# Kernel tuning notes

Measured on AMD Instinct MI355X. Metric: run time of the kernel, lower is better.

Reference implementation:

```python
import jax, jax.numpy as jnp
import numpy as np

N = 50000        # nodes
E = 500000       # edges
NUM = 4          # sampled intermediate neighbors per edge (self.num)
F = 64           # in_feats == out_feats (transform=False)
D = 32           # dist_dim
NB = 64          # embedding rows = len(boundaries)+1


def setup_inputs() -> dict:
    key = jax.random.key(0)
    ks = jax.random.split(key, 10)
    feat = jax.random.normal(ks[0], (N, F), jnp.float32)
    loc = jax.random.uniform(ks[1], (N, 3), jnp.float32)          # 3D positions in unit cube
    boundaries = jnp.sort(jax.random.uniform(ks[2], (NB - 1,), jnp.float32, 0.0, 2.0))
    embed_table = jax.random.normal(ks[3], (NB, D), jnp.float32)
    G_w = jax.random.normal(ks[4], (F, D), jnp.float32) / np.sqrt(D)      # Linear(dist_dim->out, no bias)
    agg_w = jax.random.normal(ks[5], (F, 2 * F), jnp.float32) / np.sqrt(2 * F)  # Linear(2*out->out)
    agg_b = jnp.zeros((F,), jnp.float32)
    src = jax.random.randint(ks[6], (E,), 0, N, jnp.int32)
    dst = jax.random.randint(ks[7], (E,), 0, N, jnp.int32)
    inter_ids = jax.random.randint(ks[8], (E, NUM), 0, N, jnp.int32)
    return dict(feat=feat, loc=loc, boundaries=boundaries, embed_table=embed_table,
                G_w=G_w, agg_w=agg_w, agg_b=agg_b, src=src, dst=dst, inter_ids=inter_ids)


def reference(feat, loc, boundaries, embed_table, G_w, agg_w, agg_b, src, dst, inter_ids):
    n = feat.shape[0]
    ones = jnp.ones((src.shape[0],), feat.dtype)
    # symmetric-ish degree normalization: d0 = in_deg^-0.5, d2 = out_deg^-0.5
    in_deg = jax.ops.segment_sum(ones, dst, num_segments=n)
    out_deg = jax.ops.segment_sum(ones, src, num_segments=n)
    d0 = jnp.clip(in_deg, 1.0) ** -0.5   # [N]
    d2 = jnp.clip(out_deg, 1.0) ** -0.5  # [N]

    # dist1 = ||loc[dst] - loc[src]||_2, bucketize -> embed -> G
    dist1 = jnp.linalg.norm(loc[dst] - loc[src], axis=1)              # [E]
    de1 = embed_table[jnp.searchsorted(boundaries, dist1)] @ G_w.T    # [E, F]

    # intermediate sampled neighbors: dist to each sampled node from edge src
    pos_src = loc[src]                                                # [E, 3]
    inter_pos = loc[inter_ids]                                        # [E, NUM, 3]
    dist_ = jnp.linalg.norm(pos_src[:, None, :] - inter_pos, axis=-1) # [E, NUM]
    de_ = embed_table[jnp.searchsorted(boundaries, dist_)] @ G_w.T    # [E, NUM, F]
    inter_h = feat[inter_ids]                                         # [E, NUM, F]
    dist_embed_dot_h = (de_ * inter_h).mean(axis=1)                   # [E, F]

    # h = d0[dst] * d2[src] * agg_fc([de1 * h_src, dist_embed_dot_h])
    cat = jnp.concatenate([de1 * feat[src], dist_embed_dot_h], axis=1)  # [E, 2F]
    msg = (d0[dst] * d2[src])[:, None] * (cat @ agg_w.T + agg_b)        # [E, F]

    # update_all(copy_e('h'), sum) -> scatter-sum messages to dst
    ft = jax.ops.segment_sum(msg, dst, num_segments=n)                  # [N, F]
    return ft
```

## Files before the change

kernel.cpp:

```cpp
#include <hip/hip_runtime.h>
#include <math.h>

#define LUTN 1024
#define LUTSCALE 512.0f


__global__ __launch_bounds__(256) void setup_kernel(
    const float* __restrict__ embed, const float* __restrict__ G_w,
    const float* __restrict__ boundaries, const float* __restrict__ feat,
    const float* __restrict__ loc,
    float* __restrict__ M, int* __restrict__ lut,
    int* __restrict__ d2i, int* __restrict__ cnt,
    unsigned short* __restrict__ featH, float4* __restrict__ loc4, int N) {

    const int gid = blockIdx.x * 256 + threadIdx.x;
    const int gsz = gridDim.x * 256;
    for (int i = gid; i < N; i += gsz) { cnt[i] = 0; d2i[i] = 0; }
    for (int i = gid; i < 4096; i += gsz) {
        int b = i >> 6, f = i & 63;
        float acc = 0.f;
        #pragma unroll
        for (int dd = 0; dd < 32; ++dd) acc += embed[b * 32 + dd] * G_w[f * 32 + dd];
        M[i] = acc;
    }
    for (int i = gid; i < LUTN; i += gsz) {
        float left = (float)i * (1.0f / LUTSCALE);
        int c = 0;
        for (int j = 0; j < 63; ++j) c += (boundaries[j] < left) ? 1 : 0;
        lut[i] = c;
    }
    const int nq = N * 16;
    for (int i = gid; i < nq; i += gsz) {
        float4 v = ((const float4*)feat)[i];
        unsigned ux = __float_as_uint(v.x), uy = __float_as_uint(v.y);
        unsigned uz = __float_as_uint(v.z), uw = __float_as_uint(v.w);
        ushort4 h;
        h.x = (unsigned short)((ux + 0x7FFFu + ((ux >> 16) & 1u)) >> 16);
        h.y = (unsigned short)((uy + 0x7FFFu + ((uy >> 16) & 1u)) >> 16);
        h.z = (unsigned short)((uz + 0x7FFFu + ((uz >> 16) & 1u)) >> 16);
        h.w = (unsigned short)((uw + 0x7FFFu + ((uw >> 16) & 1u)) >> 16);
        ((ushort4*)featH)[i] = h;
    }
    for (int i = gid; i < N; i += gsz)
        loc4[i] = make_float4(loc[3 * i], loc[3 * i + 1], loc[3 * i + 2], 0.f);
}


__global__ __launch_bounds__(256) void edge_kernel(
    const float4* __restrict__ loc4, const float* __restrict__ boundaries,
    const int* __restrict__ lut,
    const int* __restrict__ src, const int* __restrict__ dst,
    const int* __restrict__ inter,
    int* __restrict__ cnt, int* __restrict__ d2i,
    int4* __restrict__ recEA, int2* __restrict__ recEB, int E) {

    __shared__ int lut_s[LUTN];
    __shared__ float bl[64];
    ((int4*)lut_s)[threadIdx.x] = ((const int4*)lut)[threadIdx.x];
    if (threadIdx.x < 64)
        bl[threadIdx.x] = (threadIdx.x < 63) ? boundaries[threadIdx.x] : 3.4e38f;
    __syncthreads();

    const int e = blockIdx.x * 256 + threadIdx.x;
    if (e >= E) return;

    const int s = src[e], d = dst[e];
    const int4 ii = ((const int4*)inter)[e];

    const float4 ps = loc4[s];
    float dist[5];
    {
        float4 pd = loc4[d];
        float dx = pd.x - ps.x, dy = pd.y - ps.y, dz = pd.z - ps.z;
        dist[0] = sqrtf(dx * dx + dy * dy + dz * dz);
    }
    const int id4[4] = {ii.x, ii.y, ii.z, ii.w};
    #pragma unroll
    for (int j = 0; j < 4; ++j) {
        float4 pt = loc4[id4[j]];
        float dx = pt.x - ps.x, dy = pt.y - ps.y, dz = pt.z - ps.z;
        dist[1 + j] = sqrtf(dx * dx + dy * dy + dz * dz);
    }
    unsigned pack = 0;
    #pragma unroll
    for (int q = 0; q < 5; ++q) {
        float dq = dist[q];
        int cell = (int)(dq * LUTSCALE);
        cell = (cell > LUTN - 1) ? (LUTN - 1) : cell;
        int b = lut_s[cell];
        while (b < 63 && bl[b] < dq) ++b;
        while (b > 0 && bl[b - 1] >= dq) --b;
        pack |= ((unsigned)b) << (6 * q);
    }

    const int r = atomicAdd(&cnt[d], 1);
    atomicAdd(&d2i[s], 1);

    recEA[e] = ii;
    recEB[e] = make_int2(s | (r << 16), (int)pack);
}


__global__ __launch_bounds__(1024) void scan_block_kernel(
    const int* __restrict__ cnt, int* __restrict__ startv,
    int* __restrict__ part, int* __restrict__ d2buf, int N) {

    __shared__ int wsum[16];
    const int t = threadIdx.x, lane = t & 63, wv = t >> 6;
    const int i = blockIdx.x * 1024 + t;

    if (i < N) {
        float v = (float)d2buf[i];
        ((float*)d2buf)[i] = rsqrtf(fmaxf(v, 1.0f));
    }

    int v = (i < N) ? cnt[i] : 0;
    int x = v;
    #pragma unroll
    for (int off = 1; off < 64; off <<= 1) { int y = __shfl_up(x, off); if (lane >= off) x += y; }
    if (lane == 63) wsum[wv] = x;
    __syncthreads();
    if (t < 16) {
        int w = wsum[t], xx = w;
        #pragma unroll
        for (int off = 1; off < 16; off <<= 1) { int y = __shfl_up(xx, off); if (t >= off) xx += y; }
        wsum[t] = xx - w;
    }
    __syncthreads();
    int incl = x + wsum[wv];
    if (i < N) startv[i] = incl - v;
    if (t == 1023) part[blockIdx.x] = incl;
}

__global__ __launch_bounds__(1024) void scan_fix_kernel(
    int* __restrict__ startv, const int* __restrict__ part, int N, int nb) {

    __shared__ int po;
    if (threadIdx.x == 0) {
        int s = 0;
        for (int j = 0; j < (int)blockIdx.x; ++j) s += part[j];
        po = s;
    }
    __syncthreads();
    int i = blockIdx.x * 1024 + threadIdx.x;
    if (i < N) startv[i] += po;
}


__global__ __launch_bounds__(256) void scatter_kernel(
    const int4* __restrict__ recEA, const int2* __restrict__ recEB,
    const int* __restrict__ dst, const int* __restrict__ startv,
    const float* __restrict__ d2f, int* __restrict__ rec, int E) {

    const int e = blockIdx.x * 256 + threadIdx.x;
    if (e >= E) return;
    const int4 a = recEA[e];
    const int2 b = recEB[e];
    const int s = b.x & 0xFFFF;
    const int r = ((unsigned)b.x) >> 16;
    const int d = dst[e];
    const int pos = startv[d] + r;
    const float w = d2f[s];
    int* rp = rec + (size_t)pos * 8;
    *(int4*)(rp)     = make_int4(s, a.x, a.y, a.z);
    *(int4*)(rp + 4) = make_int4(a.w, b.y, __float_as_int(w), 0);
}


__global__ __launch_bounds__(256) void node_kernel(
    const unsigned short* __restrict__ featH, const float* __restrict__ M,
    const int* __restrict__ cnt, const int* __restrict__ startv,
    const int* __restrict__ rec, float* __restrict__ cat,
    float* __restrict__ swb, int N) {

    __shared__ float Ms[4096];
    #pragma unroll
    for (int i = 0; i < 4; ++i)
        ((float4*)Ms)[threadIdx.x + 256 * i] = ((const float4*)M)[threadIdx.x + 256 * i];
    __syncthreads();

    const int lane = threadIdx.x & 63;
    const int wid  = threadIdx.x >> 6;
    const int d    = blockIdx.x * 4 + wid;
    if (d >= N) return;

    const int deg  = __builtin_amdgcn_readfirstlane(cnt[d]);
    const int base = __builtin_amdgcn_readfirstlane(startv[d]);
    const int* rp  = rec + (size_t)base * 8;

    float acc0 = 0.f, acc1 = 0.f, sw = 0.f;

    #pragma unroll 4
    for (int k = 0; k < deg; ++k) {
        const int s  = rp[k * 8 + 0];
        const int i0 = rp[k * 8 + 1];
        const int i1 = rp[k * 8 + 2];
        const int i2 = rp[k * 8 + 3];
        const int i3 = rp[k * 8 + 4];
        const unsigned pk = (unsigned)rp[k * 8 + 5];
        const float w = __int_as_float(rp[k * 8 + 6]);

        const float fs = __uint_as_float(((unsigned)featH[(size_t)s  * 64 + lane]) << 16);
        const float f0 = __uint_as_float(((unsigned)featH[(size_t)i0 * 64 + lane]) << 16);
        const float f1 = __uint_as_float(((unsigned)featH[(size_t)i1 * 64 + lane]) << 16);
        const float f2 = __uint_as_float(((unsigned)featH[(size_t)i2 * 64 + lane]) << 16);
        const float f3 = __uint_as_float(((unsigned)featH[(size_t)i3 * 64 + lane]) << 16);
        const float m0 = Ms[(pk & 63u) * 64 + lane];
        const float m1 = Ms[((pk >> 6) & 63u) * 64 + lane];
        const float m2 = Ms[((pk >> 12) & 63u) * 64 + lane];
        const float m3 = Ms[((pk >> 18) & 63u) * 64 + lane];
        const float m4 = Ms[((pk >> 24) & 63u) * 64 + lane];

        acc0 = fmaf(m0 * fs, w, acc0);
        float t = m1 * f0 + m2 * f1 + m3 * f2 + m4 * f3;
        acc1 = fmaf(0.25f * t, w, acc1);
        sw += w;
    }

    cat[(size_t)d * 128 + lane]      = acc0;
    cat[(size_t)d * 128 + 64 + lane] = acc1;
    if (lane == 0) swb[d] = sw;
}


__global__ __launch_bounds__(256) void epilogue_kernel(
    const float* __restrict__ cat, const float* __restrict__ agg_w,
    const float* __restrict__ agg_b, const float* __restrict__ swb,
    const int* __restrict__ cnt, float* __restrict__ out, int N) {

    const int lane = threadIdx.x & 63;
    const int wid  = threadIdx.x >> 6;

    float4 aw[32];
    const float4* awp = (const float4*)(agg_w + (size_t)lane * 128);
    #pragma unroll
    for (int i = 0; i < 32; ++i) aw[i] = awp[i];
    const float bias = agg_b[lane];

    const int gw = blockIdx.x * 4 + wid;
    const int stride = gridDim.x * 4;

    for (int d0i = gw; d0i < N; d0i += stride) {
        const int du = __builtin_amdgcn_readfirstlane(d0i);
        const float* cp = cat + (size_t)du * 128;
        float a0 = bias * swb[du], a1 = 0.f, a2 = 0.f, a3 = 0.f;
        #pragma unroll
        for (int k4 = 0; k4 < 32; k4 += 4) {
            float4 c0 = ((const float4*)cp)[k4];
            float4 c1 = ((const float4*)cp)[k4 + 1];
            float4 c2 = ((const float4*)cp)[k4 + 2];
            float4 c3 = ((const float4*)cp)[k4 + 3];
            a0 = fmaf(aw[k4].x, c0.x, a0); a0 = fmaf(aw[k4].y, c0.y, a0);
            a0 = fmaf(aw[k4].z, c0.z, a0); a0 = fmaf(aw[k4].w, c0.w, a0);
            a1 = fmaf(aw[k4+1].x, c1.x, a1); a1 = fmaf(aw[k4+1].y, c1.y, a1);
            a1 = fmaf(aw[k4+1].z, c1.z, a1); a1 = fmaf(aw[k4+1].w, c1.w, a1);
            a2 = fmaf(aw[k4+2].x, c2.x, a2); a2 = fmaf(aw[k4+2].y, c2.y, a2);
            a2 = fmaf(aw[k4+2].z, c2.z, a2); a2 = fmaf(aw[k4+2].w, c2.w, a2);
            a3 = fmaf(aw[k4+3].x, c3.x, a3); a3 = fmaf(aw[k4+3].y, c3.y, a3);
            a3 = fmaf(aw[k4+3].z, c3.z, a3); a3 = fmaf(aw[k4+3].w, c3.w, a3);
        }
        const float d0v = rsqrtf(fmaxf((float)cnt[du], 1.0f));
        out[(size_t)du * 64 + lane] = d0v * ((a0 + a1) + (a2 + a3));
    }
}


extern "C" void kernel_launch(void* const* d_in, const int* in_sizes, int n_in,
                              void* d_out, int out_size, void* d_ws, size_t ws_size,
                              hipStream_t stream) {
    const float* feat       = (const float*)d_in[0];
    const float* loc        = (const float*)d_in[1];
    const float* boundaries = (const float*)d_in[2];
    const float* embed      = (const float*)d_in[3];
    const float* G_w        = (const float*)d_in[4];
    const float* agg_w      = (const float*)d_in[5];
    const float* agg_b      = (const float*)d_in[6];
    const int*   src        = (const int*)d_in[7];
    const int*   dst        = (const int*)d_in[8];
    const int*   inter      = (const int*)d_in[9];

    const int N = in_sizes[0] / 64;
    const int E = in_sizes[7];

    char* w = (char*)d_ws;
    auto take = [&](size_t bytes) { char* p = w; w += (bytes + 15) & ~(size_t)15; return p; };
    float*          M      = (float*)take(4096 * 4);
    int*            lut    = (int*)  take(LUTN * 4);
    int*            d2buf  = (int*)  take((size_t)N * 4);
    int*            cnt    = (int*)  take((size_t)N * 4);
    int*            startv = (int*)  take((size_t)N * 4);
    int*            part   = (int*)  take(256 * 4);
    int4*           recEA  = (int4*) take((size_t)E * 16);
    int2*           recEB  = (int2*) take((size_t)E * 8);
    int*            rec    = (int*)  take((size_t)E * 32);
    float*          cat    = (float*)take((size_t)N * 128 * 4);
    float*          swb    = (float*)take((size_t)N * 4);
    unsigned short* featH  = (unsigned short*)take((size_t)N * 64 * 2);
    float4*         loc4   = (float4*)take((size_t)N * 16);
    float*          out    = (float*)d_out;

    const int nb = (N + 1023) / 1024;
    const int eb = (E + 255) / 256;

    setup_kernel<<<1024, 256, 0, stream>>>(embed, G_w, boundaries, feat, loc,
                                           M, lut, d2buf, cnt, featH, loc4, N);
    edge_kernel<<<eb, 256, 0, stream>>>(loc4, boundaries, lut, src, dst, inter,
                                        cnt, d2buf, recEA, recEB, E);
    scan_block_kernel<<<nb, 1024, 0, stream>>>(cnt, startv, part, d2buf, N);
    scan_fix_kernel<<<nb, 1024, 0, stream>>>(startv, part, N, nb);
    scatter_kernel<<<eb, 256, 0, stream>>>(recEA, recEB, dst, startv,
                                           (const float*)d2buf, rec, E);
    node_kernel<<<(N + 3) / 4, 256, 0, stream>>>(featH, M, cnt, startv, rec, cat, swb, N);
    epilogue_kernel<<<768, 256, 0, stream>>>(cat, agg_w, agg_b, swb, cnt, out, N);
}
```

Before: 241.9 us.

## Pack edge records into 16 bytes and merge scan into single-block kernel

```diff
diff --git a/kernel.cpp b/kernel.cpp
--- a/kernel.cpp
+++ b/kernel.cpp
@@ -5,7 +5,7 @@
 #define LUTSCALE 512.0f
 
 
-__global__ __launch_bounds__(256) void setup_kernel(
+__global__ __launch_bounds__(256) void prep_kernel(
     const float* __restrict__ embed, const float* __restrict__ G_w,
     const float* __restrict__ boundaries, const float* __restrict__ feat,
     const float* __restrict__ loc,
@@ -52,7 +52,7 @@
     const int* __restrict__ src, const int* __restrict__ dst,
     const int* __restrict__ inter,
     int* __restrict__ cnt, int* __restrict__ d2i,
-    int4* __restrict__ recEA, int2* __restrict__ recEB, int E) {
+    int4* __restrict__ recE, int E) {
 
     __shared__ int lut_s[LUTN];
     __shared__ float bl[64];
@@ -96,26 +96,22 @@
     const int r = atomicAdd(&cnt[d], 1);
     atomicAdd(&d2i[s], 1);
 
-    recEA[e] = ii;
-    recEB[e] = make_int2(s | (r << 16), (int)pack);
-}
-
-
-__global__ __launch_bounds__(1024) void scan_block_kernel(
-    const int* __restrict__ cnt, int* __restrict__ startv,
-    int* __restrict__ part, int* __restrict__ d2buf, int N) {
+    recE[e] = make_int4(s | (ii.x << 16), ii.y | (ii.z << 16), ii.w | (r << 16), (int)pack);
+}
+
+
+__global__ __launch_bounds__(1024) void scan_kernel(
+    const int* __restrict__ cnt, int* __restrict__ startv, int N) {
 
     __shared__ int wsum[16];
     const int t = threadIdx.x, lane = t & 63, wv = t >> 6;
-    const int i = blockIdx.x * 1024 + t;
-
-    if (i < N) {
-        float v = (float)d2buf[i];
-        ((float*)d2buf)[i] = rsqrtf(fmaxf(v, 1.0f));
-    }
-
-    int v = (i < N) ? cnt[i] : 0;
-    int x = v;
+    const int C = (N + 1023) / 1024;
+    const int b0 = t * C, b1 = min(b0 + C, N);
+
+    int s = 0;
+    for (int i = b0; i < b1; ++i) s += cnt[i];
+
+    int x = s;
     #pragma unroll
     for (int off = 1; off < 64; off <<= 1) { int y = __shfl_up(x, off); if (lane >= off) x += y; }
     if (lane == 63) wsum[wv] = x;
@@ -127,50 +123,36 @@
         wsum[t] = xx - w;
     }
     __syncthreads();
-    int incl = x + wsum[wv];
-    if (i < N) startv[i] = incl - v;
-    if (t == 1023) part[blockIdx.x] = incl;
-}
-
-__global__ __launch_bounds__(1024) void scan_fix_kernel(
-    int* __restrict__ startv, const int* __restrict__ part, int N, int nb) {
-
-    __shared__ int po;
-    if (threadIdx.x == 0) {
-        int s = 0;
-        for (int j = 0; j < (int)blockIdx.x; ++j) s += part[j];
-        po = s;
-    }
-    __syncthreads();
-    int i = blockIdx.x * 1024 + threadIdx.x;
-    if (i < N) startv[i] += po;
+    int run = x + wsum[wv] - s;
+    for (int i = b0; i < b1; ++i) {
+        startv[i] = run;
+        run += cnt[i];
+    }
 }
 
 
 __global__ __launch_bounds__(256) void scatter_kernel(
-    const int4* __restrict__ recEA, const int2* __restrict__ recEB,
-    const int* __restrict__ dst, const int* __restrict__ startv,
-    const float* __restrict__ d2f, int* __restrict__ rec, int E) {
+    const int4* __restrict__ recE, const int* __restrict__ dst,
+    const int* __restrict__ startv, const int* __restrict__ d2i,
+    int4* __restrict__ rec, int E) {
 
     const int e = blockIdx.x * 256 + threadIdx.x;
     if (e >= E) return;
-    const int4 a = recEA[e];
-    const int2 b = recEB[e];
-    const int s = b.x & 0xFFFF;
-    const int r = ((unsigned)b.x) >> 16;
-    const int d = dst[e];
-    const int pos = startv[d] + r;
-    const float w = d2f[s];
-    int* rp = rec + (size_t)pos * 8;
-    *(int4*)(rp)     = make_int4(s, a.x, a.y, a.z);
-    *(int4*)(rp + 4) = make_int4(a.w, b.y, __float_as_int(w), 0);
+    const int4 a = recE[e];
+    const int s = a.x & 0xFFFF;
+    const int r = ((unsigned)a.z) >> 16;
+    const int pos = startv[dst[e]] + r;
+    const float w = rsqrtf(fmaxf((float)d2i[s], 1.0f));
+    unsigned uw = __float_as_uint(w);
+    unsigned wb = (uw + 0x7FFFu + ((uw >> 16) & 1u)) & 0xFFFF0000u;
+    rec[pos] = make_int4(a.x, a.y, (a.z & 0xFFFF) | (int)wb, a.w);
 }
 
 
 __global__ __launch_bounds__(256) void node_kernel(
     const unsigned short* __restrict__ featH, const float* __restrict__ M,
     const int* __restrict__ cnt, const int* __restrict__ startv,
-    const int* __restrict__ rec, float* __restrict__ cat,
+    const int4* __restrict__ rec, float* __restrict__ cat,
     float* __restrict__ swb, int N) {
 
     __shared__ float Ms[4096];
@@ -186,19 +168,20 @@
 
     const int deg  = __builtin_amdgcn_readfirstlane(cnt[d]);
     const int base = __builtin_amdgcn_readfirstlane(startv[d]);
-    const int* rp  = rec + (size_t)base * 8;
+    const int4* rp = rec + base;
 
     float acc0 = 0.f, acc1 = 0.f, sw = 0.f;
 
     #pragma unroll 4
     for (int k = 0; k < deg; ++k) {
-        const int s  = rp[k * 8 + 0];
-        const int i0 = rp[k * 8 + 1];
-        const int i1 = rp[k * 8 + 2];
-        const int i2 = rp[k * 8 + 3];
-        const int i3 = rp[k * 8 + 4];
-        const unsigned pk = (unsigned)rp[k * 8 + 5];
-        const float w = __int_as_float(rp[k * 8 + 6]);
+        const int4 r = rp[k];
+        const int s  = r.x & 0xFFFF;
+        const int i0 = ((unsigned)r.x) >> 16;
+        const int i1 = r.y & 0xFFFF;
+        const int i2 = ((unsigned)r.y) >> 16;
+        const int i3 = r.z & 0xFFFF;
+        const float w = __uint_as_float((unsigned)r.z & 0xFFFF0000u);
+        const unsigned pk = (unsigned)r.w;
 
         const float fs = __uint_as_float(((unsigned)featH[(size_t)s  * 64 + lane]) << 16);
         const float f0 = __uint_as_float(((unsigned)featH[(size_t)i0 * 64 + lane]) << 16);
@@ -286,30 +269,25 @@
     auto take = [&](size_t bytes) { char* p = w; w += (bytes + 15) & ~(size_t)15; return p; };
     float*          M      = (float*)take(4096 * 4);
     int*            lut    = (int*)  take(LUTN * 4);
-    int*            d2buf  = (int*)  take((size_t)N * 4);
+    int*            d2i    = (int*)  take((size_t)N * 4);
     int*            cnt    = (int*)  take((size_t)N * 4);
     int*            startv = (int*)  take((size_t)N * 4);
-    int*            part   = (int*)  take(256 * 4);
-    int4*           recEA  = (int4*) take((size_t)E * 16);
-    int2*           recEB  = (int2*) take((size_t)E * 8);
-    int*            rec    = (int*)  take((size_t)E * 32);
+    int4*           recE   = (int4*) take((size_t)E * 16);
+    int4*           rec    = (int4*) take((size_t)E * 16);
     float*          cat    = (float*)take((size_t)N * 128 * 4);
     float*          swb    = (float*)take((size_t)N * 4);
     unsigned short* featH  = (unsigned short*)take((size_t)N * 64 * 2);
     float4*         loc4   = (float4*)take((size_t)N * 16);
     float*          out    = (float*)d_out;
 
-    const int nb = (N + 1023) / 1024;
     const int eb = (E + 255) / 256;
 
-    setup_kernel<<<1024, 256, 0, stream>>>(embed, G_w, boundaries, feat, loc,
-                                           M, lut, d2buf, cnt, featH, loc4, N);
+    prep_kernel<<<1024, 256, 0, stream>>>(embed, G_w, boundaries, feat, loc,
+                                          M, lut, d2i, cnt, featH, loc4, N);
     edge_kernel<<<eb, 256, 0, stream>>>(loc4, boundaries, lut, src, dst, inter,
-                                        cnt, d2buf, recEA, recEB, E);
-    scan_block_kernel<<<nb, 1024, 0, stream>>>(cnt, startv, part, d2buf, N);
-    scan_fix_kernel<<<nb, 1024, 0, stream>>>(startv, part, N, nb);
-    scatter_kernel<<<eb, 256, 0, stream>>>(recEA, recEB, dst, startv,
-                                           (const float*)d2buf, rec, E);
+                                        cnt, d2i, recE, E);
+    scan_kernel<<<1, 1024, 0, stream>>>(cnt, startv, N);
+    scatter_kernel<<<eb, 256, 0, stream>>>(recE, dst, startv, d2i, rec, E);
     node_kernel<<<(N + 3) / 4, 256, 0, stream>>>(featH, M, cnt, startv, rec, cat, swb, N);
     epilogue_kernel<<<768, 256, 0, stream>>>(cat, agg_w, agg_b, swb, cnt, out, N);
 }
```

Measured after the change: 299.1 us. 23.6% more time.
